# Optimization experiments

Measured on AMD Instinct MI355X. Metric: run time of the kernel, lower is better.

Reference implementation:

```python
import jax, jax.numpy as jnp
import numpy as np

INPUT_DIM = 2048
N_EXPERTS = 64
K = 2


def setup_inputs() -> dict:
    key = jax.random.key(0)
    kx, kw, kb = jax.random.split(key, 3)
    x = jax.random.normal(kx, (4, 4096, INPUT_DIM), dtype=jnp.float32)
    # nn.Linear(input_dim, n_experts): weight [n_experts, input_dim], bias [n_experts]
    bound = 1.0 / np.sqrt(INPUT_DIM)
    W = jax.random.uniform(kw, (N_EXPERTS, INPUT_DIM), minval=-bound, maxval=bound, dtype=jnp.float32)
    b = jax.random.uniform(kb, (N_EXPERTS,), minval=-bound, maxval=bound, dtype=jnp.float32)
    return {"x": x, "W": W, "b": b}


def reference(x, W, b):
    # logits: [B, S, E]
    logits = jnp.einsum('bsd,ed->bse', x, W) + b
    topk_vals, topk_indices = jax.lax.top_k(logits, K)  # over last (expert) axis
    gate_probs = jax.nn.softmax(topk_vals, axis=-1)
    return gate_probs, topk_indices
```

## Files before the change

### kernel.cpp

```cpp
#include <hip/hip_runtime.h>
#include <math.h>

typedef _Float16 half8 __attribute__((ext_vector_type(8)));
typedef float floatx4 __attribute__((ext_vector_type(4)));

#define NTOK  16384
#define DIM   2048
#define NEXP  64
#define MB    16
#define NBLK  (NTOK / MB)
#define NSTEP 16
#define WSW_HALF8 (64 * 4 * 64)
#define WSW_BYTES (2 * WSW_HALF8 * 16)

__global__ void wprep_kernel(const float* __restrict__ W, _Float16* __restrict__ wsw) {
    const int id   = blockIdx.x * blockDim.x + threadIdx.x;
    const int lane = id & 63;
    const int tg   = (id >> 6) & 3;
    const int sg   = id >> 8;
    const int e    = tg * 16 + (lane & 15);
    const int k    = sg * 32 + (lane >> 4) * 8;
    const float* src = W + (size_t)e * DIM + k;
    half8 h, l;
#pragma unroll
    for (int j = 0; j < 8; j++) {
        const float v  = src[j];
        const _Float16 hh = (_Float16)v;
        h[j] = hh;
        l[j] = (_Float16)((v - (float)hh) * 2048.0f);
    }
    const size_t slot = (size_t)(sg * 4 + tg) * 64 + lane;
    ((half8*)wsw)[slot]             = h;
    ((half8*)wsw)[WSW_HALF8 + slot] = l;
}

__device__ __forceinline__ void split_a(const float4& v0, const float4& v1,
                                        half8& hi, half8& lo) {
    const float av[8] = {v0.x, v0.y, v0.z, v0.w, v1.x, v1.y, v1.z, v1.w};
#pragma unroll
    for (int j = 0; j < 8; j++) {
        const _Float16 hh = (_Float16)av[j];
        hi[j] = hh;
        lo[j] = (_Float16)((av[j] - (float)hh) * 2048.0f);
    }
}

template <bool USE_WS>
__global__ __launch_bounds__(256, 4)
void gating_mfma_kernel(const float* __restrict__ x, const float* __restrict__ W,
                        const _Float16* __restrict__ wsw, const float* __restrict__ bias,
                        float* __restrict__ out)
{
    __shared__ float part[4 * MB * 65];

    const int tid  = threadIdx.x;
    const int lane = tid & 63;
    const int kh   = tid >> 6;
    const int col  = lane & 15;
    const int quad = lane >> 4;
    const int tok0 = blockIdx.x * MB;

    const float* xrow = x + (size_t)(tok0 + col) * DIM + kh * 512 + quad * 8;
    const half8* bh_base = (const half8*)wsw + (size_t)kh * 4096 + lane;
    const half8* bl_base = bh_base + WSW_HALF8;

    floatx4 accm[4] = {{0,0,0,0},{0,0,0,0},{0,0,0,0},{0,0,0,0}};
    floatx4 accl[4] = {{0,0,0,0},{0,0,0,0},{0,0,0,0},{0,0,0,0}};

    float4 xf[2][2];
    half8  bhf[2][4], blf[2][4];

    xf[0][0] = *(const float4*)(xrow);
    xf[0][1] = *(const float4*)(xrow + 4);
    xf[1][0] = *(const float4*)(xrow + 32);
    xf[1][1] = *(const float4*)(xrow + 36);
    if constexpr (USE_WS) {
#pragma unroll
        for (int tg = 0; tg < 4; tg++) { bhf[0][tg] = bh_base[tg * 64]; blf[0][tg] = bl_base[tg * 64]; }
    } else {
#pragma unroll
        for (int tg = 0; tg < 4; tg++) {
            const float* wr = W + (size_t)(tg * 16 + col) * DIM + kh * 512 + quad * 8;
            split_a(*(const float4*)(wr), *(const float4*)(wr + 4), bhf[0][tg], blf[0][tg]);
        }
    }

#pragma unroll
    for (int s = 0; s < NSTEP; ++s) {
        const int cur = s & 1, nxt = cur ^ 1;

        half8 ah, alo;
        split_a(xf[cur][0], xf[cur][1], ah, alo);

        if (s + 2 < NSTEP) {
            xf[cur][0] = *(const float4*)(xrow + (s + 2) * 32);
            xf[cur][1] = *(const float4*)(xrow + (s + 2) * 32 + 4);
        }
        if (s + 1 < NSTEP) {
            if constexpr (USE_WS) {
#pragma unroll
                for (int tg = 0; tg < 4; tg++) {
                    bhf[nxt][tg] = bh_base[(s + 1) * 256 + tg * 64];
                    blf[nxt][tg] = bl_base[(s + 1) * 256 + tg * 64];
                }
            } else {
#pragma unroll
                for (int tg = 0; tg < 4; tg++) {
                    const float* wr = W + (size_t)(tg * 16 + col) * DIM + kh * 512 + (s + 1) * 32 + quad * 8;
                    split_a(*(const float4*)(wr), *(const float4*)(wr + 4), bhf[nxt][tg], blf[nxt][tg]);
                }
            }
        }

#pragma unroll
        for (int tg = 0; tg < 4; tg++) {
            accm[tg] = __builtin_amdgcn_mfma_f32_16x16x32_f16(ah,  bhf[cur][tg], accm[tg], 0, 0, 0);
            accl[tg] = __builtin_amdgcn_mfma_f32_16x16x32_f16(ah,  blf[cur][tg], accl[tg], 0, 0, 0);
            accl[tg] = __builtin_amdgcn_mfma_f32_16x16x32_f16(alo, bhf[cur][tg], accl[tg], 0, 0, 0);
        }
    }

    const float inv = 1.0f / 2048.0f;
#pragma unroll
    for (int tg = 0; tg < 4; tg++) {
#pragma unroll
        for (int r = 0; r < 4; r++) {
            const int m = quad * 4 + r;
            part[(kh * MB + m) * 65 + tg * 16 + col] = accm[tg][r] + accl[tg][r] * inv;
        }
    }
    __syncthreads();

    if (tid < MB) {
        const int t = tid;
        float v0 = -INFINITY, v1 = -INFINITY;
        int   i0 = 0, i1 = 0;
        for (int e = 0; e < NEXP; e++) {
            const float v = part[t * 65 + e] + part[(MB + t) * 65 + e]
                          + part[(2 * MB + t) * 65 + e] + part[(3 * MB + t) * 65 + e]
                          + bias[e];
            if (v > v0) { v1 = v0; i1 = i0; v0 = v; i0 = e; }
            else if (v > v1) { v1 = v; i1 = e; }
        }
        const float e1 = expf(v1 - v0);
        const float sden = 1.f + e1;
        const int   g  = tok0 + t;
        out[2 * g + 0] = 1.f / sden;
        out[2 * g + 1] = e1 / sden;
        out[2 * NTOK + 2 * g + 0] = (float)i0;
        out[2 * NTOK + 2 * g + 1] = (float)i1;
    }
}

extern "C" void kernel_launch(void* const* d_in, const int* in_sizes, int n_in,
                              void* d_out, int out_size, void* d_ws, size_t ws_size,
                              hipStream_t stream) {
    const float* x    = (const float*)d_in[0];
    const float* W    = (const float*)d_in[1];
    const float* bias = (const float*)d_in[2];
    float*       out  = (float*)d_out;
    _Float16*    wsw  = (_Float16*)d_ws;

    if (ws_size >= (size_t)WSW_BYTES) {
        hipLaunchKernelGGL(wprep_kernel, dim3(64), dim3(256), 0, stream, (const float*)d_in[1], wsw);
        hipLaunchKernelGGL((gating_mfma_kernel<true>), dim3(NBLK), dim3(256), 0, stream,
                           x, W, wsw, bias, out);
    } else {
        hipLaunchKernelGGL((gating_mfma_kernel<false>), dim3(NBLK), dim3(256), 0, stream,
                           x, W, wsw, bias, out);
    }
}
```

Baseline: 219.9 us.

## Stage x and split weights through double-buffered LDS with direct global-to-LDS loads

Replaces the per-wave K-split register pipeline with a 32-token block that streams 64-wide K chunks of x and the prepared fp16 hi/lo weights into double-buffered LDS using global_load_lds DMA, using an XOR swizzle to avoid bank conflicts. Waves now split over token tiles and expert halves instead of K, so the cross-wave partial-sum reduction disappears. The aim is to cut redundant weight traffic per token and overlap loads with MFMA work. In exchange it adds a barrier per chunk, uses more shared memory, and lowers the occupancy bound to 3 blocks.

```diff
diff --git a/kernel.cpp b/kernel.cpp
--- a/kernel.cpp
+++ b/kernel.cpp
@@ -1,17 +1,25 @@
 #include <hip/hip_runtime.h>
 #include <math.h>
+#include <stdint.h>
 
 typedef _Float16 half8 __attribute__((ext_vector_type(8)));
 typedef float floatx4 __attribute__((ext_vector_type(4)));
 
-#define NTOK  16384
-#define DIM   2048
-#define NEXP  64
-#define MB    16
-#define NBLK  (NTOK / MB)
-#define NSTEP 16
-#define WSW_HALF8 (64 * 4 * 64)
-#define WSW_BYTES (2 * WSW_HALF8 * 16)
+#define NTOK   16384
+#define DIM    2048
+#define NEXP   64
+#define MB     32
+#define NBLK   (NTOK / MB)
+#define KC     64
+#define NCHUNK (DIM / KC)
+#define WSW_H8 16384
+#define WSW_BYTES (2 * WSW_H8 * 16)
+
+#define A_BYTES 8192
+#define B_BYTES 16384
+#define AOFF(b) ((b) * A_BYTES)
+#define BOFF(b) (2 * A_BYTES + (b) * B_BYTES)
+#define SMEM_BYTES (2 * A_BYTES + 2 * B_BYTES)
 
 __global__ void wprep_kernel(const float* __restrict__ W, _Float16* __restrict__ wsw) {
     const int id   = blockIdx.x * blockDim.x + threadIdx.x;
@@ -30,8 +38,8 @@
         l[j] = (_Float16)((v - (float)hh) * 2048.0f);
     }
     const size_t slot = (size_t)(sg * 4 + tg) * 64 + lane;
-    ((half8*)wsw)[slot]             = h;
-    ((half8*)wsw)[WSW_HALF8 + slot] = l;
+    ((half8*)wsw)[slot]          = h;
+    ((half8*)wsw)[WSW_H8 + slot] = l;
 }
 
 __device__ __forceinline__ void split_a(const float4& v0, const float4& v1,
@@ -45,88 +53,113 @@
     }
 }
 
+__device__ __forceinline__ void dma16(const void* g, const char* l) {
+    __builtin_amdgcn_global_load_lds(
+        (const __attribute__((address_space(1))) unsigned int*)(uintptr_t)g,
+        (__attribute__((address_space(3))) unsigned int*)(uintptr_t)l,
+        16, 0, 0);
+}
+
 template <bool USE_WS>
-__global__ __launch_bounds__(256, 4)
-void gating_mfma_kernel(const float* __restrict__ x, const float* __restrict__ W,
-                        const _Float16* __restrict__ wsw, const float* __restrict__ bias,
-                        float* __restrict__ out)
+__global__ __launch_bounds__(256, 3)
+void gating_lds_kernel(const float* __restrict__ x, const float* __restrict__ W,
+                       const _Float16* __restrict__ wsw, const float* __restrict__ bias,
+                       float* __restrict__ out)
 {
-    __shared__ float part[4 * MB * 65];
+    __shared__ char smem[SMEM_BYTES];
 
     const int tid  = threadIdx.x;
     const int lane = tid & 63;
-    const int kh   = tid >> 6;
+    const int w    = tid >> 6;
+    const int mt   = w & 1;
+    const int nh   = w >> 1;
     const int col  = lane & 15;
     const int quad = lane >> 4;
     const int tok0 = blockIdx.x * MB;
-
-    const float* xrow = x + (size_t)(tok0 + col) * DIM + kh * 512 + quad * 8;
-    const half8* bh_base = (const half8*)wsw + (size_t)kh * 4096 + lane;
-    const half8* bl_base = bh_base + WSW_HALF8;
-
-    floatx4 accm[4] = {{0,0,0,0},{0,0,0,0},{0,0,0,0},{0,0,0,0}};
-    floatx4 accl[4] = {{0,0,0,0},{0,0,0,0},{0,0,0,0},{0,0,0,0}};
-
-    float4 xf[2][2];
-    half8  bhf[2][4], blf[2][4];
-
-    xf[0][0] = *(const float4*)(xrow);
-    xf[0][1] = *(const float4*)(xrow + 4);
-    xf[1][0] = *(const float4*)(xrow + 32);
-    xf[1][1] = *(const float4*)(xrow + 36);
+    const int m    = mt * 16 + col;
+
+    const float* gA[2];
+    unsigned     lA[2];
+#pragma unroll
+    for (int i = 0; i < 2; i++) {
+        const int a   = w * 2 + i;
+        const int row = a * 4 + (lane >> 4);
+        const int pz  = lane & 15;
+        const int gp  = (pz & 8) | ((pz & 7) ^ (row & 7));
+        gA[i] = x + (size_t)(tok0 + row) * DIM + gp * 4;
+        lA[i] = (unsigned)(a * 1024);
+    }
+    const half8* gB[4];
+    unsigned     lB[4];
     if constexpr (USE_WS) {
 #pragma unroll
-        for (int tg = 0; tg < 4; tg++) { bhf[0][tg] = bh_base[tg * 64]; blf[0][tg] = bl_base[tg * 64]; }
-    } else {
-#pragma unroll
-        for (int tg = 0; tg < 4; tg++) {
-            const float* wr = W + (size_t)(tg * 16 + col) * DIM + kh * 512 + quad * 8;
-            split_a(*(const float4*)(wr), *(const float4*)(wr + 4), bhf[0][tg], blf[0][tg]);
-        }
-    }
-
-#pragma unroll
-    for (int s = 0; s < NSTEP; ++s) {
-        const int cur = s & 1, nxt = cur ^ 1;
-
-        half8 ah, alo;
-        split_a(xf[cur][0], xf[cur][1], ah, alo);
-
-        if (s + 2 < NSTEP) {
-            xf[cur][0] = *(const float4*)(xrow + (s + 2) * 32);
-            xf[cur][1] = *(const float4*)(xrow + (s + 2) * 32 + 4);
-        }
-        if (s + 1 < NSTEP) {
+        for (int j = 0; j < 4; j++) {
+            const int b = w * 4 + j;
+            const int split = b >> 3, idx = b & 7;
+            gB[j] = (const half8*)wsw + (size_t)split * WSW_H8 + idx * 64 + lane;
+            lB[j] = (unsigned)(split * 8192 + idx * 1024);
+        }
+    }
+
+    floatx4 accm[2] = {{0,0,0,0},{0,0,0,0}};
+    floatx4 accl[2] = {{0,0,0,0},{0,0,0,0}};
+
+#pragma unroll
+    for (int i = 0; i < 2; i++) dma16(gA[i], smem + AOFF(0) + lA[i]);
+    if constexpr (USE_WS) {
+#pragma unroll
+        for (int j = 0; j < 4; j++) dma16(gB[j], smem + BOFF(0) + lB[j]);
+    }
+
+#pragma unroll 2
+    for (int c = 0; c < NCHUNK; ++c) {
+        __syncthreads();
+        if (c + 1 < NCHUNK) {
+            const int nb = (c + 1) & 1;
+#pragma unroll
+            for (int i = 0; i < 2; i++)
+                dma16(gA[i] + (size_t)(c + 1) * KC, smem + AOFF(nb) + lA[i]);
             if constexpr (USE_WS) {
 #pragma unroll
-                for (int tg = 0; tg < 4; tg++) {
-                    bhf[nxt][tg] = bh_base[(s + 1) * 256 + tg * 64];
-                    blf[nxt][tg] = bl_base[(s + 1) * 256 + tg * 64];
+                for (int j = 0; j < 4; j++)
+                    dma16(gB[j] + (size_t)(c + 1) * 512, smem + BOFF(nb) + lB[j]);
+            }
+        }
+        const char* Ab = smem + AOFF(c & 1);
+        const char* Bb = smem + BOFF(c & 1);
+#pragma unroll
+        for (int s = 0; s < 2; s++) {
+            const float4 v0 = *(const float4*)(Ab + m * 256 + (8 * s + ((2 * quad + 0) ^ (m & 7))) * 16);
+            const float4 v1 = *(const float4*)(Ab + m * 256 + (8 * s + ((2 * quad + 1) ^ (m & 7))) * 16);
+            half8 ah, alo;
+            split_a(v0, v1, ah, alo);
+#pragma unroll
+            for (int t = 0; t < 2; t++) {
+                const int tg = nh * 2 + t;
+                half8 bh, bl;
+                if constexpr (USE_WS) {
+                    bh = *(const half8*)(Bb + (s * 4 + tg) * 1024 + lane * 16);
+                    bl = *(const half8*)(Bb + 8192 + (s * 4 + tg) * 1024 + lane * 16);
+                } else {
+                    const float* wr = W + (size_t)(tg * 16 + col) * DIM + c * KC + s * 32 + quad * 8;
+                    split_a(*(const float4*)wr, *(const float4*)(wr + 4), bh, bl);
                 }
-            } else {
-#pragma unroll
-                for (int tg = 0; tg < 4; tg++) {
-                    const float* wr = W + (size_t)(tg * 16 + col) * DIM + kh * 512 + (s + 1) * 32 + quad * 8;
-                    split_a(*(const float4*)(wr), *(const float4*)(wr + 4), bhf[nxt][tg], blf[nxt][tg]);
-                }
+                accm[t] = __builtin_amdgcn_mfma_f32_16x16x32_f16(ah,  bh, accm[t], 0, 0, 0);
+                accl[t] = __builtin_amdgcn_mfma_f32_16x16x32_f16(ah,  bl, accl[t], 0, 0, 0);
+                accl[t] = __builtin_amdgcn_mfma_f32_16x16x32_f16(alo, bh, accl[t], 0, 0, 0);
             }
         }
-
-#pragma unroll
-        for (int tg = 0; tg < 4; tg++) {
-            accm[tg] = __builtin_amdgcn_mfma_f32_16x16x32_f16(ah,  bhf[cur][tg], accm[tg], 0, 0, 0);
-            accl[tg] = __builtin_amdgcn_mfma_f32_16x16x32_f16(ah,  blf[cur][tg], accl[tg], 0, 0, 0);
-            accl[tg] = __builtin_amdgcn_mfma_f32_16x16x32_f16(alo, bhf[cur][tg], accl[tg], 0, 0, 0);
-        }
-    }
-
+    }
+
+    __syncthreads();
+    float* lg = (float*)smem;
     const float inv = 1.0f / 2048.0f;
 #pragma unroll
-    for (int tg = 0; tg < 4; tg++) {
+    for (int t = 0; t < 2; t++) {
+        const int tg = nh * 2 + t;
 #pragma unroll
         for (int r = 0; r < 4; r++) {
-            const int m = quad * 4 + r;
-            part[(kh * MB + m) * 65 + tg * 16 + col] = accm[tg][r] + accl[tg][r] * inv;
+            lg[(mt * 16 + quad * 4 + r) * 65 + tg * 16 + col] = accm[t][r] + accl[t][r] * inv;
         }
     }
     __syncthreads();
@@ -136,9 +169,7 @@
         float v0 = -INFINITY, v1 = -INFINITY;
         int   i0 = 0, i1 = 0;
         for (int e = 0; e < NEXP; e++) {
-            const float v = part[t * 65 + e] + part[(MB + t) * 65 + e]
-                          + part[(2 * MB + t) * 65 + e] + part[(3 * MB + t) * 65 + e]
-                          + bias[e];
+            const float v = lg[t * 65 + e] + bias[e];
             if (v > v0) { v1 = v0; i1 = i0; v0 = v; i0 = e; }
             else if (v > v1) { v1 = v; i1 = e; }
         }
@@ -163,10 +194,10 @@
 
     if (ws_size >= (size_t)WSW_BYTES) {
         hipLaunchKernelGGL(wprep_kernel, dim3(64), dim3(256), 0, stream, (const float*)d_in[1], wsw);
-        hipLaunchKernelGGL((gating_mfma_kernel<true>), dim3(NBLK), dim3(256), 0, stream,
+        hipLaunchKernelGGL((gating_lds_kernel<true>), dim3(NBLK), dim3(256), 0, stream,
                            x, W, wsw, bias, out);
     } else {
-        hipLaunchKernelGGL((gating_mfma_kernel<false>), dim3(NBLK), dim3(256), 0, stream,
+        hipLaunchKernelGGL((gating_lds_kernel<false>), dim3(NBLK), dim3(256), 0, stream,
                            x, W, wsw, bias, out);
     }
 }
```

Result: faster. 208.1 us (-5.4%).

## Raise token tile to 32 with 8-wave K split and vectorized LDS reduction

Applied to the files above, without the earlier changes.

Each block now handles 32 tokens with 512 threads. Each of the 8 waves owns a 256-wide K slice and computes two 16-token M tiles, so every loaded W fragment is reused across twice as many tokens and global W traffic per token is halved. The old rolling register double-buffer is replaced by batched loads of two K steps followed by a sched_barrier and then the MFMAs. The cross-wave partial sums are reduced with vectorized LDS reads, and the bias is added before the per-token top-2. The costs are more registers per thread, less explicit load/compute overlap, and a larger LDS footprint.

```diff
diff --git a/kernel.cpp b/kernel.cpp
--- a/kernel.cpp
+++ b/kernel.cpp
@@ -1,17 +1,18 @@
 #include <hip/hip_runtime.h>
 #include <math.h>
+#include <stdint.h>
 
 typedef _Float16 half8 __attribute__((ext_vector_type(8)));
 typedef float floatx4 __attribute__((ext_vector_type(4)));
 
-#define NTOK  16384
-#define DIM   2048
-#define NEXP  64
-#define MB    16
-#define NBLK  (NTOK / MB)
-#define NSTEP 16
-#define WSW_HALF8 (64 * 4 * 64)
-#define WSW_BYTES (2 * WSW_HALF8 * 16)
+#define NTOK 16384
+#define DIM  2048
+#define NEXP 64
+#define MB   32
+#define NBLK (NTOK / MB)
+#define THREADS 512
+#define WSW_H8 16384
+#define WSW_BYTES (2 * WSW_H8 * 16)
 
 __global__ void wprep_kernel(const float* __restrict__ W, _Float16* __restrict__ wsw) {
     const int id   = blockIdx.x * blockDim.x + threadIdx.x;
@@ -30,8 +31,8 @@
         l[j] = (_Float16)((v - (float)hh) * 2048.0f);
     }
     const size_t slot = (size_t)(sg * 4 + tg) * 64 + lane;
-    ((half8*)wsw)[slot]             = h;
-    ((half8*)wsw)[WSW_HALF8 + slot] = l;
+    ((half8*)wsw)[slot]          = h;
+    ((half8*)wsw)[WSW_H8 + slot] = l;
 }
 
 __device__ __forceinline__ void split_a(const float4& v0, const float4& v1,
@@ -46,88 +47,102 @@
 }
 
 template <bool USE_WS>
-__global__ __launch_bounds__(256, 4)
-void gating_mfma_kernel(const float* __restrict__ x, const float* __restrict__ W,
+__global__ __launch_bounds__(THREADS, 2)
+void gating_regB_kernel(const float* __restrict__ x, const float* __restrict__ W,
                         const _Float16* __restrict__ wsw, const float* __restrict__ bias,
                         float* __restrict__ out)
 {
-    __shared__ float part[4 * MB * 65];
+    __shared__ __align__(16) float part[8 * MB * 64];
 
     const int tid  = threadIdx.x;
     const int lane = tid & 63;
-    const int kh   = tid >> 6;
+    const int w    = tid >> 6;
     const int col  = lane & 15;
     const int quad = lane >> 4;
     const int tok0 = blockIdx.x * MB;
+    const int sg0  = w * 8;
 
-    const float* xrow = x + (size_t)(tok0 + col) * DIM + kh * 512 + quad * 8;
-    const half8* bh_base = (const half8*)wsw + (size_t)kh * 4096 + lane;
-    const half8* bl_base = bh_base + WSW_HALF8;
+    floatx4 accm[2][4], accl[2][4];
+#pragma unroll
+    for (int m = 0; m < 2; m++)
+#pragma unroll
+        for (int tg = 0; tg < 4; tg++) { accm[m][tg] = {0,0,0,0}; accl[m][tg] = {0,0,0,0}; }
 
-    floatx4 accm[4] = {{0,0,0,0},{0,0,0,0},{0,0,0,0},{0,0,0,0}};
-    floatx4 accl[4] = {{0,0,0,0},{0,0,0,0},{0,0,0,0},{0,0,0,0}};
+    const half8* bb    = (const half8*)wsw + lane;
+    const float* xbase = x + (size_t)tok0 * DIM + quad * 8;
 
-    float4 xf[2][2];
-    half8  bhf[2][4], blf[2][4];
+    for (int ss = 0; ss < 4; ++ss) {
+        const int sgA = sg0 + 2 * ss;
 
-    xf[0][0] = *(const float4*)(xrow);
-    xf[0][1] = *(const float4*)(xrow + 4);
-    xf[1][0] = *(const float4*)(xrow + 32);
-    xf[1][1] = *(const float4*)(xrow + 36);
-    if constexpr (USE_WS) {
+        half8 bh[2][4], bl[2][4];
+        if constexpr (USE_WS) {
 #pragma unroll
-        for (int tg = 0; tg < 4; tg++) { bhf[0][tg] = bh_base[tg * 64]; blf[0][tg] = bl_base[tg * 64]; }
-    } else {
+            for (int s2 = 0; s2 < 2; ++s2)
 #pragma unroll
-        for (int tg = 0; tg < 4; tg++) {
-            const float* wr = W + (size_t)(tg * 16 + col) * DIM + kh * 512 + quad * 8;
-            split_a(*(const float4*)(wr), *(const float4*)(wr + 4), bhf[0][tg], blf[0][tg]);
+                for (int tg = 0; tg < 4; ++tg) {
+                    const size_t fi = (size_t)((sgA + s2) * 4 + tg) * 64;
+                    bh[s2][tg] = bb[fi];
+                    bl[s2][tg] = bb[WSW_H8 + fi];
+                }
+        } else {
+#pragma unroll
+            for (int s2 = 0; s2 < 2; ++s2)
+#pragma unroll
+                for (int tg = 0; tg < 4; ++tg) {
+                    const float* wr = W + (size_t)(tg * 16 + col) * DIM + (sgA + s2) * 32 + quad * 8;
+                    split_a(*(const float4*)wr, *(const float4*)(wr + 4), bh[s2][tg], bl[s2][tg]);
+                }
         }
-    }
+        float4 av[2][2][2];
+#pragma unroll
+        for (int m = 0; m < 2; ++m)
+#pragma unroll
+            for (int s2 = 0; s2 < 2; ++s2) {
+                const float* ap = xbase + (size_t)(m * 16 + col) * DIM + (sgA + s2) * 32;
+                av[m][s2][0] = *(const float4*)(ap);
+                av[m][s2][1] = *(const float4*)(ap + 4);
+            }
+
+        __builtin_amdgcn_sched_barrier(0);
 
 #pragma unroll
-    for (int s = 0; s < NSTEP; ++s) {
-        const int cur = s & 1, nxt = cur ^ 1;
-
-        half8 ah, alo;
-        split_a(xf[cur][0], xf[cur][1], ah, alo);
-
-        if (s + 2 < NSTEP) {
-            xf[cur][0] = *(const float4*)(xrow + (s + 2) * 32);
-            xf[cur][1] = *(const float4*)(xrow + (s + 2) * 32 + 4);
-        }
-        if (s + 1 < NSTEP) {
-            if constexpr (USE_WS) {
+        for (int m = 0; m < 2; ++m)
 #pragma unroll
-                for (int tg = 0; tg < 4; tg++) {
-                    bhf[nxt][tg] = bh_base[(s + 1) * 256 + tg * 64];
-                    blf[nxt][tg] = bl_base[(s + 1) * 256 + tg * 64];
-                }
-            } else {
+            for (int s2 = 0; s2 < 2; ++s2) {
+                half8 ah, al;
+                split_a(av[m][s2][0], av[m][s2][1], ah, al);
 #pragma unroll
-                for (int tg = 0; tg < 4; tg++) {
-                    const float* wr = W + (size_t)(tg * 16 + col) * DIM + kh * 512 + (s + 1) * 32 + quad * 8;
-                    split_a(*(const float4*)(wr), *(const float4*)(wr + 4), bhf[nxt][tg], blf[nxt][tg]);
+                for (int tg = 0; tg < 4; ++tg) {
+                    accm[m][tg] = __builtin_amdgcn_mfma_f32_16x16x32_f16(ah, bh[s2][tg], accm[m][tg], 0, 0, 0);
+                    accl[m][tg] = __builtin_amdgcn_mfma_f32_16x16x32_f16(ah, bl[s2][tg], accl[m][tg], 0, 0, 0);
+                    accl[m][tg] = __builtin_amdgcn_mfma_f32_16x16x32_f16(al, bh[s2][tg], accl[m][tg], 0, 0, 0);
                 }
             }
-        }
-
-#pragma unroll
-        for (int tg = 0; tg < 4; tg++) {
-            accm[tg] = __builtin_amdgcn_mfma_f32_16x16x32_f16(ah,  bhf[cur][tg], accm[tg], 0, 0, 0);
-            accl[tg] = __builtin_amdgcn_mfma_f32_16x16x32_f16(ah,  blf[cur][tg], accl[tg], 0, 0, 0);
-            accl[tg] = __builtin_amdgcn_mfma_f32_16x16x32_f16(alo, bhf[cur][tg], accl[tg], 0, 0, 0);
-        }
     }
 
     const float inv = 1.0f / 2048.0f;
 #pragma unroll
-    for (int tg = 0; tg < 4; tg++) {
+    for (int m = 0; m < 2; ++m)
 #pragma unroll
-        for (int r = 0; r < 4; r++) {
-            const int m = quad * 4 + r;
-            part[(kh * MB + m) * 65 + tg * 16 + col] = accm[tg][r] + accl[tg][r] * inv;
-        }
+        for (int tg = 0; tg < 4; ++tg)
+#pragma unroll
+            for (int r = 0; r < 4; ++r)
+                part[w * 2048 + (m * 16 + quad * 4 + r) * 64 + tg * 16 + col]
+                    = accm[m][tg][r] + accl[m][tg][r] * inv;
+    __syncthreads();
+
+    floatx4 red = {0, 0, 0, 0};
+#pragma unroll
+    for (int w2 = 0; w2 < 8; ++w2)
+        red += *(const floatx4*)(part + w2 * 2048 + tid * 4);
+    const floatx4 bv = *(const floatx4*)(bias + ((tid * 4) & 63));
+    __syncthreads();
+
+    float* fin = part;
+#pragma unroll
+    for (int i = 0; i < 4; ++i) {
+        const int p = tid * 4 + i;
+        fin[(p >> 6) * 65 + (p & 63)] = red[i] + bv[i];
     }
     __syncthreads();
 
@@ -136,9 +151,7 @@
         float v0 = -INFINITY, v1 = -INFINITY;
         int   i0 = 0, i1 = 0;
         for (int e = 0; e < NEXP; e++) {
-            const float v = part[t * 65 + e] + part[(MB + t) * 65 + e]
-                          + part[(2 * MB + t) * 65 + e] + part[(3 * MB + t) * 65 + e]
-                          + bias[e];
+            const float v = fin[t * 65 + e];
             if (v > v0) { v1 = v0; i1 = i0; v0 = v; i0 = e; }
             else if (v > v1) { v1 = v; i1 = e; }
         }
@@ -163,10 +176,10 @@
 
     if (ws_size >= (size_t)WSW_BYTES) {
         hipLaunchKernelGGL(wprep_kernel, dim3(64), dim3(256), 0, stream, (const float*)d_in[1], wsw);
-        hipLaunchKernelGGL((gating_mfma_kernel<true>), dim3(NBLK), dim3(256), 0, stream,
+        hipLaunchKernelGGL((gating_regB_kernel<true>), dim3(NBLK), dim3(THREADS), 0, stream,
                            x, W, wsw, bias, out);
     } else {
-        hipLaunchKernelGGL((gating_mfma_kernel<false>), dim3(NBLK), dim3(256), 0, stream,
+        hipLaunchKernelGGL((gating_regB_kernel<false>), dim3(NBLK), dim3(THREADS), 0, stream,
                            x, W, wsw, bias, out);
     }
 }
```

After: 213.2 us. 1.03x faster.
